# Kernel tuning notes

Measured on AMD Instinct MI355X. Metric: run time of the kernel, lower is better.

## Reference

```python
import jax, jax.numpy as jnp
import numpy as np

MAX_FREQ = 10
CORR_RADIUS = 2
PATCH = 9


def _gelu(x):
    return jax.nn.gelu(x, approximate=False)


def _project(coords, R, C0, f, pp):
    # coords [N,3] -> uv [ncams,N,2], cam-space z [ncams,N]
    d = coords[None, :, :] - C0[:, None, :]
    Xc = jnp.einsum('cij,cnj->cni', R, d)
    z = jnp.maximum(Xc[..., 2:3], 1e-6)
    uv = Xc[..., :2] / z * f[:, None, :] + pp[:, None, :]
    return uv, Xc[..., 2]


def _fourier(x, max_freq):
    freqs = (2.0 ** jnp.arange(max_freq, dtype=x.dtype)) * jnp.pi
    xf = x[..., None] * freqs
    enc = jnp.concatenate([jnp.sin(xf), jnp.cos(xf)], axis=-1)  # [...,D,2F]
    return enc.reshape(enc.shape[:-2] + (x.shape[-1] * 2 * max_freq,))


def _bilinear_time(img, t, gx, gy):
    # img [B,T,C,H,W]; t [B,K] int; gx,gy [B,K,P] normalized grid in [-1,1]
    # grid_sample(align_corners=False, padding_mode='zeros') via direct 4-tap gather
    B, T, C, H, W = img.shape
    x = (gx + 1.0) * 0.5 * W - 0.5
    y = (gy + 1.0) * 0.5 * H - 0.5
    x0 = jnp.floor(x)
    y0 = jnp.floor(y)
    wx = (x - x0)[..., None]
    wy = (y - y0)[..., None]
    x0 = x0.astype(jnp.int32)
    y0 = y0.astype(jnp.int32)
    b = jnp.arange(B)[:, None, None]
    tt = t[:, :, None]

    def tap(yy, xx):
        ok = ((xx >= 0) & (xx < W) & (yy >= 0) & (yy < H))[..., None]
        v = img[b, tt, :, jnp.clip(yy, 0, H - 1), jnp.clip(xx, 0, W - 1)]  # [B,K,P,C]
        return v * ok.astype(v.dtype)

    return (tap(y0, x0) * (1 - wx) * (1 - wy) + tap(y0, x0 + 1) * wx * (1 - wy)
            + tap(y0 + 1, x0) * (1 - wx) * wy + tap(y0 + 1, x0 + 1) * wx * wy)


def _conv2d(x, w, b):
    y = jax.lax.conv_general_dilated(x, w, (1, 1), 'SAME', dimension_numbers=('NCHW', 'OIHW', 'NCHW'))
    return y + b[None, :, None, None]


def _conv3d(x, w, b):
    y = jax.lax.conv_general_dilated(x, w, (1, 1, 1), 'SAME', dimension_numbers=('NCDHW', 'OIDHW', 'NCDHW'))
    return y + b[None, :, None, None, None]


def reference(views, cam_R, cam_center, cam_focal, cam_pp, query_coords, query_time, target_time, cube_scale, v2v_w, v2v_b, lin_vol_w, lin_vol_b, lin_pos_w, lin_pos_b, lin_depth_w, lin_depth_b, conv1_w, conv1_b, conv2_w, conv2_b, conv3_w, conv3_b, mlp1_w, mlp1_b, mlp2_w, mlp2_b, tq_emb, tt_emb, vis_emb_tab, depth_norm_scale, gate_w, gate_b, fus1_w, fus1_b, fus2_w, fus2_b):
    ncams, B, T, C, H, W = views.shape
    K = query_coords.shape[1]
    sizes = jnp.asarray([W, H], dtype=query_coords.dtype)

    # project query points to all cameras
    qflat = query_coords.reshape(-1, 3)
    p2d_flat, zc = _project(qflat, cam_R, cam_center, cam_focal, cam_pp)  # [ncams,BK,2]
    p2d_full = p2d_flat.reshape(ncams, B, K, 2)

    # fourier position embedding
    pp_n = jnp.transpose(p2d_full, (1, 2, 0, 3)) / sizes  # [B,K,ncams,2]
    embed_pos = _fourier(pp_n, MAX_FREQ) @ lin_pos_w.T + lin_pos_b

    # volume embedding: masked multi-camera cube sampling + 3D conv
    cs = 2 * CORR_RADIUS + 1
    P3 = cs ** 3
    row = (jnp.arange(cs, dtype=query_coords.dtype) - CORR_RADIUS) * (cube_scale * 2.0)
    gx3, gy3, gz3 = jnp.meshgrid(row, row, row, indexing='ij')
    xyz = jnp.stack([gx3, gy3, gz3], axis=-1).reshape(-1, 3)  # [P3,3], x outermost
    cube = (query_coords[:, :, None, :] + xyz).reshape(-1, 3)
    pc, _ = _project(cube, cam_R, cam_center, cam_focal, cam_pp)
    pc = pc.reshape(ncams, B, K, P3, 2)
    smps, msks = [], []
    for c in range(ncams):
        g = 2.0 * pc[c] / sizes - 1.0
        m = (g[..., 0] >= -1) & (g[..., 0] <= 1) & (g[..., 1] >= -1) & (g[..., 1] <= 1)
        s = _bilinear_time(views[c], query_time, g[..., 0], g[..., 1])  # [B,K,P3,C]
        smps.append(s)
        msks.append(m)
    vol = jnp.stack(smps)  # [ncams,B,K,P3,C]
    mf = jnp.stack(msks).astype(vol.dtype)[..., None]
    cnt = jnp.maximum(mf.sum(0), 1.0)
    mv = (vol * mf).sum(0) / cnt  # [B,K,P3,C]
    mv = mv.reshape(B, K, cs, cs, cs, C)  # (x,y,z,C)
    mv = jnp.transpose(mv, (0, 1, 5, 4, 3, 2)).reshape(B * K, C, cs, cs, cs)  # [(BK),C,z,y,x]
    mv = _gelu(_conv3d(mv, v2v_w, v2v_b))  # EmbedV2V: Conv3d(3,vdim,3) + GELU
    vd = mv.shape[1]
    mv = mv.reshape(B, K, vd, cs, cs, cs)
    mv = jnp.transpose(mv, (0, 1, 2, 5, 4, 3)).reshape(B, K, vd * P3)  # 'b t 1 (d total)'
    embed_volume = mv @ lin_vol_w.T + lin_vol_b
    embed_volume = jnp.broadcast_to(embed_volume[:, :, None, :], (B, K, ncams, embed_volume.shape[-1]))

    # patch embedding per camera
    lin = jnp.arange(PATCH, dtype=query_coords.dtype)
    gyy, gxx = jnp.meshgrid(lin, lin, indexing='ij')
    offs = jnp.stack([gxx - (PATCH - 1) / 2.0, gyy - (PATCH - 1) / 2.0], axis=-1)  # [P,P,2]
    pats = []
    for c in range(ncams):
        px = p2d_full[c][:, :, None, None, :] + offs  # [B,K,P,P,2]
        g = ((2.0 * px + 1.0) / sizes - 1.0).reshape(B, K, PATCH * PATCH, 2)
        s = _bilinear_time(views[c], query_time, g[..., 0], g[..., 1])  # [B,K,PP,C]
        pats.append(jnp.transpose(s.reshape(B, K, PATCH, PATCH, C), (0, 1, 4, 2, 3)))
    patches = jnp.stack(pats).reshape(ncams * B * K, C, PATCH, PATCH)
    x = _gelu(_conv2d(patches, conv1_w, conv1_b))
    x = _gelu(_conv2d(x, conv2_w, conv2_b))
    x = _gelu(_conv2d(x, conv3_w, conv3_b))
    x = x.reshape(x.shape[0], -1)  # 'b c p q -> b (c p q)'
    x = _gelu(x @ mlp1_w.T + mlp1_b)  # dropout is eval-mode identity
    emb_p = x @ mlp2_w.T + mlp2_b
    embed_patch = jnp.transpose(emb_p.reshape(ncams, B, K, -1), (1, 2, 0, 3))

    E = tq_emb.shape[1]
    embed_qt = jnp.broadcast_to(tq_emb[query_time][:, :, None, :], (B, K, ncams, E))
    embed_tt = jnp.broadcast_to(tt_emb[target_time][:, :, None, :], (B, K, ncams, E))

    # visibility (pinhole in-bounds check with margin=2)
    u = p2d_flat[..., 0]
    v = p2d_flat[..., 1]
    margin = 2.0
    vis = (zc > 0) & (u >= margin) & (u <= W - margin) & (v >= margin) & (v <= H - margin)
    vis = jnp.transpose(vis.reshape(ncams, B, K), (1, 2, 0))  # [B,K,ncams]
    embed_vis = vis_emb_tab[vis.astype(jnp.int32)]

    depths = jnp.linalg.norm(query_coords[:, :, None, :] - cam_center, axis=-1) / (cube_scale * depth_norm_scale[0])
    embed_depth = _fourier(depths[..., None], MAX_FREQ) @ lin_depth_w.T + lin_depth_b

    # gated fusion of 7 terms + fusion MLP
    terms = [embed_pos, embed_volume, embed_patch, embed_qt, embed_tt, embed_vis, embed_depth]
    gates = jax.nn.sigmoid(jnp.concatenate(terms, axis=-1) @ gate_w.T + gate_b)  # [B,K,ncams,7]
    fused = sum(gates[..., i:i + 1] * terms[i] for i in range(len(terms)))
    h = _gelu(fused @ fus1_w.T + fus1_b)
    embed_total = h @ fus2_w.T + fus2_b  # [B,K,ncams,decoder_dim]
    return embed_total, vis


def setup_inputs():
    ks = jax.random.split(jax.random.key(0), 24)
    ncams, B, T, C, H, W = 4, 2, 16, 3, 256, 256
    K, E, MF, cs, P, vdim = 256, 256, 10, 5, 9, 8
    views = jax.random.normal(ks[0], (ncams, B, T, C, H, W), jnp.float32)
    cam_R = jnp.tile(jnp.eye(3, dtype=jnp.float32)[None], (ncams, 1, 1))
    cam_center = jnp.stack([jnp.linspace(-0.5, 0.5, ncams), jnp.linspace(0.5, -0.5, ncams), jnp.full((ncams,), -5.0)], axis=-1).astype(jnp.float32)
    cam_focal = jnp.full((ncams, 2), 200.0, jnp.float32)
    cam_pp = jnp.full((ncams, 2), 128.0, jnp.float32)
    query_coords = jax.random.uniform(ks[1], (B, K, 3), jnp.float32, -1.0, 1.0)
    query_time = jax.random.randint(ks[2], (B, K), 0, T).astype(jnp.int32)
    target_time = jax.random.randint(ks[3], (B, K), 0, T).astype(jnp.int32)
    cube_scale = jnp.float32(0.02)

    def w(k, shape, s=0.02):
        return jax.random.normal(k, shape, jnp.float32) * s

    z = lambda n: jnp.zeros((n,), jnp.float32)
    return dict(
        views=views, cam_R=cam_R, cam_center=cam_center, cam_focal=cam_focal, cam_pp=cam_pp,
        query_coords=query_coords, query_time=query_time, target_time=target_time, cube_scale=cube_scale,
        v2v_w=w(ks[4], (vdim, C, 3, 3, 3)), v2v_b=z(vdim),
        lin_vol_w=w(ks[5], (E, cs ** 3 * vdim)), lin_vol_b=z(E),
        lin_pos_w=w(ks[6], (E, 4 * MF)), lin_pos_b=z(E),
        lin_depth_w=w(ks[7], (E, 2 * MF)), lin_depth_b=z(E),
        conv1_w=w(ks[8], (32, 3, 3, 3)), conv1_b=z(32),
        conv2_w=w(ks[9], (64, 32, 3, 3)), conv2_b=z(64),
        conv3_w=w(ks[10], (128, 64, 3, 3)), conv3_b=z(128),
        mlp1_w=w(ks[11], (2 * E, 128 * P * P)), mlp1_b=z(2 * E),
        mlp2_w=w(ks[12], (E, 2 * E)), mlp2_b=z(E),
        tq_emb=w(ks[13], (T, E), 1.0), tt_emb=w(ks[14], (T, E), 1.0),
        vis_emb_tab=w(ks[15], (2, E), 1.0),
        depth_norm_scale=jnp.array([500.0], jnp.float32),
        gate_w=w(ks[16], (7, 7 * E), 0.01), gate_b=z(7),
        fus1_w=w(ks[17], (4 * E, E)), fus1_b=z(4 * E),
        fus2_w=w(ks[18], (E, 4 * E)), fus2_b=z(E),
    )
```

## Files before the change

kernel.cpp:

```cpp
#include <hip/hip_runtime.h>
#include <hip/hip_bf16.h>

typedef __hip_bfloat16 bf16;
typedef __attribute__((ext_vector_type(8))) short short8;
typedef __attribute__((ext_vector_type(4))) float floatx4;

#define NC 4
#define BB 2
#define TS 16
#define CHN 3
#define HH 256
#define WW 256
#define KQ 256
#define EE 256
#define BKT 512
#define HW 65536
#define IMG_CHUNK 1024
#define NSEG 27
#define CH1 32
#define CH1P 40
#define CH2 64
#define CH2P 72
#define PW 11

#define PB_WCL   32
#define PB_W23   160
#define PB_AUXW  416
#define PB_PROJ  424
#define PB_CUBE  936
#define PB_END   1960

__device__ __forceinline__ float tof(bf16 x){ return __bfloat162float(x); }
__device__ __forceinline__ bf16 tobf(float x){ return __float2bfloat16(x); }
__device__ __forceinline__ float gelu_f(float x){ return 0.5f*x*(1.f+erff(x*0.70710678118654752f)); }
__device__ __forceinline__ float ldx(const void* p, size_t i, int bf){
    return bf ? tof(((const bf16*)p)[i]) : ((const float*)p)[i];
}
__device__ __forceinline__ void gload_lds16(const void* g, void* l){
    __builtin_amdgcn_global_load_lds((const __attribute__((address_space(1))) void*)g,
                                     (__attribute__((address_space(3))) void*)l, 16, 0, 0);
}

struct CvtArgs { const void* src[NSEG]; int dstoff[NSEG]; int cnt[NSEG]; };

struct PrepArgs {
    const void *camF, *camR, *camC, *camP, *qc, *csc;
    const void *c2w, *c3w, *linv, *f1w, *f2w, *m2w, *m1w, *views;
    const int* qtime;
    bf16 *w2cl, *w3cl, *linv_bf, *f1w_bf, *f2w_bf, *m2w_bf, *m1w_bf;
    float *p2d, *visf, *mv;
    void* dout;
    int* flagp;
};

__global__ __launch_bounds__(256) void prep_kernel(CvtArgs ca, float* __restrict__ pool, PrepArgs a)
{
    int bid = blockIdx.x, tid = threadIdx.x;
    int bf = (((const unsigned short*)a.camF)[0] != 0) ? 1 : 0;

    if (bid < PB_WCL){
        for (int s=0; s<NSEG; ++s){
            const void* src = ca.src[s];
            float* d = pool + ca.dstoff[s];
            int n = ca.cnt[s];
            for (int i = bid*256 + tid; i < n; i += PB_WCL*256) d[i] = ldx(src, i, bf);
        }
    } else if (bid < PB_W23){
        int i0 = (bid-PB_WCL)*256 + tid;
        const int stride = (PB_W23-PB_WCL)*256;
        for (int i=i0; i<64*32*9; i+=stride){
            int oc=i/(32*9), r=i%(32*9), ic=r/9, tap=r%9;
            a.w2cl[tap*(64*CH1) + oc*CH1 + ic] = tobf(ldx(a.c2w, i, bf));
        }
        for (int i=i0; i<128*64*9; i+=stride){
            int oc=i/(64*9), r=i%(64*9), ic=r/9, tap=r%9;
            a.w3cl[tap*(128*CH2) + oc*CH2 + ic] = tobf(ldx(a.c3w, i, bf));
        }
    } else if (bid < PB_AUXW){
        int sub = (bid-PB_W23)>>6;
        int i0 = ((bid-PB_W23)&63)*256 + tid;
        const int stride = 64*256;
        if (sub==0){
            for (int i=i0; i<256*1024; i+=stride){
                int r=i>>10, c=i&1023;
                a.linv_bf[i] = tobf(c<1000 ? ldx(a.linv, (size_t)r*1000+c, bf) : 0.f);
            }
        } else if (sub==1){
            for (int i=i0; i<1024*256; i+=stride) a.f1w_bf[i]=tobf(ldx(a.f1w,i,bf));
        } else if (sub==2){
            for (int i=i0; i<256*1024; i+=stride) a.f2w_bf[i]=tobf(ldx(a.f2w,i,bf));
        } else {
            for (int i=i0; i<256*512; i+=stride) a.m2w_bf[i]=tobf(ldx(a.m2w,i,bf));
        }
    } else if (bid < PB_PROJ){
        if (bid==PB_AUXW && tid==0) *a.flagp = bf;
        int idx = (bid-PB_AUXW)*256 + tid;
        if (idx < NC*BKT){
            int c = idx / BKT, bk = idx % BKT;
            float dx = ldx(a.qc,bk*3+0,bf) - ldx(a.camC,c*3+0,bf);
            float dy = ldx(a.qc,bk*3+1,bf) - ldx(a.camC,c*3+1,bf);
            float dz = ldx(a.qc,bk*3+2,bf) - ldx(a.camC,c*3+2,bf);
            float X0 = ldx(a.camR,c*9+0,bf)*dx + ldx(a.camR,c*9+1,bf)*dy + ldx(a.camR,c*9+2,bf)*dz;
            float X1 = ldx(a.camR,c*9+3,bf)*dx + ldx(a.camR,c*9+4,bf)*dy + ldx(a.camR,c*9+5,bf)*dz;
            float X2 = ldx(a.camR,c*9+6,bf)*dx + ldx(a.camR,c*9+7,bf)*dy + ldx(a.camR,c*9+8,bf)*dz;
            float z = fmaxf(X2, 1e-6f);
            float u = X0/z*ldx(a.camF,c*2+0,bf) + ldx(a.camP,c*2+0,bf);
            float v = X1/z*ldx(a.camF,c*2+1,bf) + ldx(a.camP,c*2+1,bf);
            a.p2d[idx*2+0] = u; a.p2d[idx*2+1] = v;
            bool vis = (X2 > 0.f) && (u >= 2.f) && (u <= (float)WW-2.f) && (v >= 2.f) && (v <= (float)HH-2.f);
            a.visf[idx] = vis ? 1.f : 0.f;
            float vv = vis ? 1.f : 0.f;
            size_t vidx = (size_t)BB*KQ*NC*EE + (size_t)bk*NC + c;
            if (bf) ((bf16*)a.dout)[vidx] = tobf(vv);
            else    ((float*)a.dout)[vidx] = vv;
        }
    } else if (bid < PB_CUBE){
        int bk = bid - PB_PROJ;
        int c = tid & 3;
        int pg = tid >> 2;
        int b = bk >> 8;
        float cs2 = ldx(a.csc,0,bf) * 2.f;
        int t = a.qtime[bk];
        float qx0 = ldx(a.qc,bk*3+0,bf);
        float qy0 = ldx(a.qc,bk*3+1,bf);
        float qz0 = ldx(a.qc,bk*3+2,bf);
        float R0=ldx(a.camR,c*9+0,bf), R1=ldx(a.camR,c*9+1,bf), R2=ldx(a.camR,c*9+2,bf);
        float R3=ldx(a.camR,c*9+3,bf), R4=ldx(a.camR,c*9+4,bf), R5=ldx(a.camR,c*9+5,bf);
        float R6=ldx(a.camR,c*9+6,bf), R7=ldx(a.camR,c*9+7,bf), R8=ldx(a.camR,c*9+8,bf);
        float Cx=ldx(a.camC,c*3+0,bf), Cy=ldx(a.camC,c*3+1,bf), Cz=ldx(a.camC,c*3+2,bf);
        float Fx=ldx(a.camF,c*2+0,bf), Fy=ldx(a.camF,c*2+1,bf);
        float Px=ldx(a.camP,c*2+0,bf), Py=ldx(a.camP,c*2+1,bf);
        #pragma unroll
        for (int pass=0; pass<2; ++pass){
            int p = (pass<<6) + pg;
            bool act = p < 125;
            float a0=0.f,a1=0.f,a2=0.f,ms=0.f;
            if (act){
                int i=p/25, j=(p/5)%5, kz=p%5;
                float qx = qx0 + (float)(i-2)*cs2;
                float qy = qy0 + (float)(j-2)*cs2;
                float qz = qz0 + (float)(kz-2)*cs2;
                float dx=qx-Cx, dy=qy-Cy, dz=qz-Cz;
                float X0=R0*dx+R1*dy+R2*dz;
                float X1=R3*dx+R4*dy+R5*dz;
                float X2=R6*dx+R7*dy+R8*dz;
                float z = fmaxf(X2,1e-6f);
                float u = X0/z*Fx+Px, v = X1/z*Fy+Py;
                if (u>=0.f && u<=(float)WW && v>=0.f && v<=(float)HH){
                    ms = 1.f;
                    float x = u-0.5f, y = v-0.5f;
                    float xf = floorf(x), yf = floorf(y);
                    int ix=(int)xf, iy=(int)yf;
                    float wx=x-xf, wy=y-yf;
                    size_t basev = (size_t)((c*BB+b)*TS + t)*CHN*HW;
                    float wxs[2]={1.f-wx,wx}, wys[2]={1.f-wy,wy};
                    #pragma unroll
                    for (int ty=0;ty<2;++ty){
                        int yy=iy+ty; if (yy<0||yy>=HH) continue;
                        #pragma unroll
                        for (int tx=0;tx<2;++tx){
                            int xx=ix+tx; if (xx<0||xx>=WW) continue;
                            float wt=wys[ty]*wxs[tx];
                            size_t o = basev + (size_t)yy*WW+xx;
                            a0 += wt*ldx(a.views,o,bf);
                            a1 += wt*ldx(a.views,o+HW,bf);
                            a2 += wt*ldx(a.views,o+2*HW,bf);
                        }
                    }
                }
            }
            a0 += __shfl_xor(a0,1); a0 += __shfl_xor(a0,2);
            a1 += __shfl_xor(a1,1); a1 += __shfl_xor(a1,2);
            a2 += __shfl_xor(a2,1); a2 += __shfl_xor(a2,2);
            ms += __shfl_xor(ms,1); ms += __shfl_xor(ms,2);
            if (act && c==0){
                float cnt = fmaxf(ms,1.f);
                a.mv[(bk*125+p)*3+0]=a0/cnt;
                a.mv[(bk*125+p)*3+1]=a1/cnt;
                a.mv[(bk*125+p)*3+2]=a2/cnt;
            }
        }
    } else {
        int i0 = (bid-PB_CUBE)*256 + tid;
        const int stride = (PB_END-PB_CUBE)*256;
        const int npair = (512*10368)/2;
        if (bf){
            const unsigned* s = (const unsigned*)a.m1w;
            unsigned* d = (unsigned*)a.m1w_bf;
            for (int i=i0; i<npair; i+=stride) d[i] = s[i];
        } else {
            const float2* s = (const float2*)a.m1w;
            unsigned* d = (unsigned*)a.m1w_bf;
            for (int i=i0; i<npair; i+=stride){
                float2 v = s[i];
                union { bf16 h[2]; unsigned u; } pk;
                pk.h[0]=tobf(v.x); pk.h[1]=tobf(v.y);
                d[i] = pk.u;
            }
        }
    }
}

__global__ __launch_bounds__(128) void vol_conv3d_kernel(
    const float* __restrict__ mv, const float* __restrict__ w,
    const float* __restrict__ bias, bf16* __restrict__ outb)
{
    int bk = blockIdx.x; int tid = threadIdx.x;
    __shared__ float vol[3][7][7][7];
    __shared__ float ws[648];
    __shared__ float bs[8];
    for (int idx=tid; idx<3*343; idx+=128) ((float*)vol)[idx]=0.f;
    for (int idx=tid; idx<648; idx+=128) ws[idx]=w[idx];
    if (tid<8) bs[tid]=bias[tid];
    __syncthreads();
    if (tid<125){
        int i=tid/25, j=(tid/5)%5, kz=tid%5;
        #pragma unroll
        for (int ch=0;ch<3;++ch) vol[ch][kz+1][j+1][i+1] = mv[(bk*125+tid)*3+ch];
    }
    __syncthreads();
    if (tid >= 104 && tid < 128) outb[bk*1024 + 1000 + (tid-104)] = tobf(0.f);
    if (tid<125){
        int w2=tid/25, h2=(tid/5)%5, d2=tid%5;
        for (int oc=0;oc<8;++oc){
            float acc = bs[oc];
            #pragma unroll
            for (int ic=0;ic<3;++ic)
              #pragma unroll
              for (int dz=0;dz<3;++dz)
                #pragma unroll
                for (int dy=0;dy<3;++dy)
                  #pragma unroll
                  for (int dxx=0;dxx<3;++dxx)
                    acc += vol[ic][d2+dz][h2+dy][w2+dxx] * ws[(((oc*3+ic)*3+dz)*3+dy)*3+dxx];
            outb[bk*1024 + oc*125 + tid] = tobf(gelu_f(acc));
        }
    }
}

__global__ __launch_bounds__(256) void patchconv_mfma_kernel(
    const void* __restrict__ views, const float* __restrict__ p2d,
    const int* __restrict__ qtime,
    const float* __restrict__ w1, const float* __restrict__ b1,
    const bf16* __restrict__ w2cl, const float* __restrict__ b2,
    const bf16* __restrict__ w3cl, const float* __restrict__ b3,
    bf16* __restrict__ act_out, int img0, const int* __restrict__ flagp)
{
    int img = img0 + blockIdx.x;
    int c = img>>9, b = (img>>8)&1, k = img&255;
    int bk = b*KQ + k;
    int tid = threadIdx.x;
    int wave = tid>>6, lane = tid&63;

    __shared__ __align__(16) bf16 a2cl[11*PW*CH2P];
    __shared__ __align__(16) bf16 a1cl[11*PW*CH1P];
    __shared__ float w1s[864];
    __shared__ float patch[3][11][11];

    for (int i=tid;i<3*11*11;i+=256) ((float*)patch)[i]=0.f;
    for (int i=tid;i<864;i+=256) w1s[i]=w1[i];
    {
        unsigned int* z1=(unsigned int*)a1cl; int n1 = 11*PW*CH1P/2;
        for (int i=tid;i<n1;i+=256) z1[i]=0u;
        unsigned int* z2=(unsigned int*)a2cl; int n2 = 11*PW*CH2P/2;
        for (int i=tid;i<n2;i+=256) z2[i]=0u;
    }
    __syncthreads();
    if (tid<243){
        int bf = *flagp;
        int ch = tid/81;
        int pp = tid - ch*81;
        float u=p2d[(c*BKT+bk)*2+0], v=p2d[(c*BKT+bk)*2+1];
        int t=qtime[bk];
        int r=pp/9,q=pp%9;
        float x=u+(float)(q-4), y=v+(float)(r-4);
        float xf=floorf(x), yf=floorf(y);
        int ix=(int)xf, iy=(int)yf;
        float wx=x-xf, wy=y-yf;
        size_t base = (size_t)((c*BB+b)*TS+t)*CHN*HW + (size_t)ch*HW;
        float acc=0.f;
        float wxs[2]={1.f-wx,wx}, wys[2]={1.f-wy,wy};
        #pragma unroll
        for (int ty=0;ty<2;++ty){
            int yy=iy+ty; if (yy<0||yy>=HH) continue;
            #pragma unroll
            for (int tx=0;tx<2;++tx){
                int xx=ix+tx; if (xx<0||xx>=WW) continue;
                acc += wys[ty]*wxs[tx]*ldx(views, base + (size_t)yy*WW+xx, bf);
            }
        }
        patch[ch][r+1][q+1]=acc;
    }
    __syncthreads();
    for (int o=tid;o<81*32;o+=256){
        int oc=o&31, pp=o>>5;
        int r=pp/9, q=pp-9*r;
        float acc=b1[oc];
        #pragma unroll
        for (int ic=0;ic<3;++ic)
          #pragma unroll
          for (int dy2=0;dy2<3;++dy2)
            #pragma unroll
            for (int dx2=0;dx2<3;++dx2)
              acc += patch[ic][r+dy2][q+dx2]*w1s[((oc*3+ic)*3+dy2)*3+dx2];
        a1cl[((r+1)*PW+(q+1))*CH1P + oc] = tobf(gelu_f(acc));
    }
    __syncthreads();
    int mrow = lane&15;
    int kgrp = lane>>4;
    int koff = kgrp<<3;
    {
        int baseoff[6];
        #pragma unroll
        for (int m=0;m<6;++m){
            int pos = m*16 + mrow; if (pos>80) pos=80;
            int r=pos/9, q=pos-9*r;
            baseoff[m] = (r*PW+q)*CH1P + koff;
        }
        floatx4 acc2[6];
        #pragma unroll
        for (int m=0;m<6;++m) acc2[m]=(floatx4){0.f,0.f,0.f,0.f};
        int n0 = wave<<4;
        #pragma unroll
        for (int tap=0; tap<9; ++tap){
            int dy=tap/3, dx=tap-3*dy;
            short8 bfrag = *(const short8*)(w2cl + ((size_t)tap*64 + n0 + mrow)*CH1 + koff);
            int toff = (dy*PW+dx)*CH1P;
            #pragma unroll
            for (int m=0;m<6;++m){
                short8 afrag = *(const short8*)&a1cl[baseoff[m]+toff];
                acc2[m] = __builtin_amdgcn_mfma_f32_16x16x32_bf16(afrag, bfrag, acc2[m], 0,0,0);
            }
        }
        int oc = n0 + mrow;
        float bb = b2[oc];
        #pragma unroll
        for (int m=0;m<6;++m){
            #pragma unroll
            for (int rg=0;rg<4;++rg){
                int pos = m*16 + (kgrp<<2)+rg;
                if (pos<=80){
                    int r=pos/9,q=pos-9*r;
                    a2cl[((r+1)*PW+(q+1))*CH2P + oc] = tobf(gelu_f(acc2[m][rg]+bb));
                }
            }
        }
    }
    __syncthreads();
    {
        int baseoff[6];
        #pragma unroll
        for (int m=0;m<6;++m){
            int pos = m*16 + mrow; if (pos>80) pos=80;
            int r=pos/9, q=pos-9*r;
            baseoff[m] = (r*PW+q)*CH2P;
        }
        floatx4 acc3[2][6];
        #pragma unroll
        for (int nt=0;nt<2;++nt)
          #pragma unroll
          for (int m=0;m<6;++m) acc3[nt][m]=(floatx4){0.f,0.f,0.f,0.f};
        int n0 = wave<<5;
        #pragma unroll
        for (int tap=0; tap<9; ++tap){
            int dy=tap/3, dx=tap-3*dy;
            int toff = (dy*PW+dx)*CH2P;
            #pragma unroll
            for (int ks=0;ks<2;++ks){
                int kof2 = (ks<<5) + koff;
                short8 b0 = *(const short8*)(w3cl + ((size_t)tap*128 + n0      + mrow)*CH2 + kof2);
                short8 b1f= *(const short8*)(w3cl + ((size_t)tap*128 + n0 + 16 + mrow)*CH2 + kof2);
                #pragma unroll
                for (int m=0;m<6;++m){
                    short8 af = *(const short8*)&a2cl[baseoff[m]+toff+kof2];
                    acc3[0][m] = __builtin_amdgcn_mfma_f32_16x16x32_bf16(af, b0,  acc3[0][m], 0,0,0);
                    acc3[1][m] = __builtin_amdgcn_mfma_f32_16x16x32_bf16(af, b1f, acc3[1][m], 0,0,0);
                }
            }
        }
        #pragma unroll
        for (int nt=0;nt<2;++nt){
            int oc = n0 + (nt<<4) + mrow;
            float bb = b3[oc];
            #pragma unroll
            for (int m=0;m<6;++m){
                #pragma unroll
                for (int rg=0;rg<4;++rg){
                    int pos = m*16 + (kgrp<<2)+rg;
                    if (pos<=80)
                        act_out[(size_t)blockIdx.x*10368 + oc*81 + pos] = tobf(gelu_f(acc3[nt][m][rg]+bb));
                }
            }
        }
    }
}

template<int OUT>
__global__ __launch_bounds__(256) void gemm_bf16_kernel(
    const bf16* __restrict__ A, const bf16* __restrict__ W, const float* __restrict__ bias,
    float* __restrict__ Cf, void* __restrict__ Cb, int M, int N, int K, int iters,
    const int* __restrict__ flagp)
{
    __shared__ bf16 As[2][64][72];
    __shared__ bf16 Bs[2][64][72];
    int tid = threadIdx.x;
    int wave = tid>>6, lane = tid&63;
    int m0 = blockIdx.y<<6, n0 = blockIdx.x<<6;
    int bfflag = (OUT==3) ? *flagp : 0;
    int lr = tid>>3;
    int lc = (tid&7)<<3;
    const bf16* Ap0 = A + (size_t)(m0+lr)*K    + lc;
    const bf16* Ap1 = A + (size_t)(m0+lr+32)*K + lc;
    const bf16* Wp0 = W + (size_t)(n0+lr)*K    + lc;
    const bf16* Wp1 = W + (size_t)(n0+lr+32)*K + lc;
    uint4 ra0 = *(const uint4*)Ap0;
    uint4 ra1 = *(const uint4*)Ap1;
    uint4 rb0 = *(const uint4*)Wp0;
    uint4 rb1 = *(const uint4*)Wp1;
    floatx4 acc[4];
    #pragma unroll
    for (int j=0;j<4;++j) acc[j] = (floatx4){0.f,0.f,0.f,0.f};
    int arow = (wave<<4) + (lane&15);
    int koff = (lane>>4)<<3;
    int nrow = lane&15;
    *(uint4*)&As[0][lr][lc]    = ra0;
    *(uint4*)&As[0][lr+32][lc] = ra1;
    *(uint4*)&Bs[0][lr][lc]    = rb0;
    *(uint4*)&Bs[0][lr+32][lc] = rb1;
    __syncthreads();
    for (int it=0; it<iters; ++it){
        int cur = it&1;
        if (it+1<iters){
            int off = (it+1)<<6;
            ra0 = *(const uint4*)(Ap0+off);
            ra1 = *(const uint4*)(Ap1+off);
            rb0 = *(const uint4*)(Wp0+off);
            rb1 = *(const uint4*)(Wp1+off);
        }
        #pragma unroll
        for (int kk=0; kk<64; kk+=32){
            short8 af = *(const short8*)&As[cur][arow][kk+koff];
            #pragma unroll
            for (int j=0;j<4;++j){
                short8 bfr = *(const short8*)&Bs[cur][(j<<4)+nrow][kk+koff];
                acc[j] = __builtin_amdgcn_mfma_f32_16x16x32_bf16(af, bfr, acc[j], 0, 0, 0);
            }
        }
        if (it+1<iters){
            __syncthreads();
            int nxt = cur^1;
            *(uint4*)&As[nxt][lr][lc]    = ra0;
            *(uint4*)&As[nxt][lr+32][lc] = ra1;
            *(uint4*)&Bs[nxt][lr][lc]    = rb0;
            *(uint4*)&Bs[nxt][lr+32][lc] = rb1;
            __syncthreads();
        }
    }
    int crow = (wave<<4) + ((lane>>4)<<2);
    int ccol = lane&15;
    #pragma unroll
    for (int j=0;j<4;++j){
        int n = n0 + (j<<4) + ccol;
        if (OUT==1){
            float bb = bias[n];
            #pragma unroll
            for (int r=0;r<4;++r)
                ((bf16*)Cb)[(size_t)(m0+crow+r)*N + n] = tobf(gelu_f(acc[j][r] + bb));
        } else if (OUT==2){
            #pragma unroll
            for (int r=0;r<4;++r)
                Cf[(size_t)(m0+crow+r)*N + n] = acc[j][r];
        } else {
            float bb = bias[n];
            #pragma unroll
            for (int r=0;r<4;++r){
                float v = acc[j][r] + bb;
                size_t ii = (size_t)(m0+crow+r)*N + n;
                if (bfflag) ((bf16*)Cb)[ii] = tobf(v);
                else        ((float*)Cb)[ii] = v;
            }
        }
    }
}

__global__ __launch_bounds__(256) void gemm128_kernel(
    const bf16* __restrict__ A, const bf16* __restrict__ W,
    float* __restrict__ Cf, int N, int K, int kiters_total, int zdiv, int pstride)
{
    __shared__ __align__(16) bf16 As[128][64];
    __shared__ __align__(16) bf16 Bs[128][64];
    int tid = threadIdx.x;
    int wave = tid>>6, lane = tid&63;
    int m0 = blockIdx.y<<7, n0 = blockIdx.x<<7;
    int it0 = (int)(((long)blockIdx.z     * kiters_total) / zdiv);
    int it1 = (int)(((long)(blockIdx.z+1) * kiters_total) / zdiv);
    float* out = Cf + (size_t)blockIdx.z * pstride;
    int srow = (wave<<5) + (lane>>3);
    int scol = (lane&7)<<3;
    const bf16* Ap = A + (size_t)(m0+srow)*K + ((size_t)it0<<6) + scol;
    const bf16* Bp = W + (size_t)(n0+srow)*K + ((size_t)it0<<6) + scol;
    bf16* AsW = &As[wave<<5][0];
    bf16* BsW = &Bs[wave<<5][0];
    floatx4 acc[4][4];
    #pragma unroll
    for (int i=0;i<4;++i)
      #pragma unroll
      for (int j=0;j<4;++j) acc[i][j] = (floatx4){0.f,0.f,0.f,0.f};
    int wm = (wave>>1)<<6, wn = (wave&1)<<6;
    int frow = lane&15, koff = (lane>>4)<<3;
    for (int it=it0; it<it1; ++it){
        size_t off = (size_t)(it-it0)<<6;
        #pragma unroll
        for (int j=0;j<4;++j){
            gload_lds16(Ap + (size_t)(j<<3)*K + off, AsW + (j<<3)*64);
            gload_lds16(Bp + (size_t)(j<<3)*K + off, BsW + (j<<3)*64);
        }
        __syncthreads();
        #pragma unroll
        for (int kk=0;kk<64;kk+=32){
            short8 af[4], bfv[4];
            #pragma unroll
            for (int i=0;i<4;++i) af[i]  = *(const short8*)&As[wm + (i<<4) + frow][kk+koff];
            #pragma unroll
            for (int j=0;j<4;++j) bfv[j] = *(const short8*)&Bs[wn + (j<<4) + frow][kk+koff];
            #pragma unroll
            for (int i=0;i<4;++i)
              #pragma unroll
              for (int j=0;j<4;++j)
                acc[i][j] = __builtin_amdgcn_mfma_f32_16x16x32_bf16(af[i], bfv[j], acc[i][j], 0,0,0);
        }
        __syncthreads();
    }
    int crow = (lane>>4)<<2;
    int ccol = lane&15;
    #pragma unroll
    for (int i=0;i<4;++i){
        int mrow = m0 + wm + (i<<4) + crow;
        #pragma unroll
        for (int j=0;j<4;++j){
            int n = n0 + wn + (j<<4) + ccol;
            #pragma unroll
            for (int r=0;r<4;++r)
                out[(size_t)(mrow+r)*N + n] = acc[i][j][r];
        }
    }
}

__global__ __launch_bounds__(256) void mlp1_fin_kernel(const float* __restrict__ P,
                                                       const float* __restrict__ bias,
                                                       bf16* __restrict__ Cb, int total, int Nmask,
                                                       int pstride){
    for (int i = blockIdx.x*256 + threadIdx.x; i < total; i += gridDim.x*256){
        float s = bias[i & Nmask];
        #pragma unroll
        for (int p=0;p<8;++p) s += P[(size_t)p*pstride + i];
        Cb[i] = tobf(gelu_f(s));
    }
}

__global__ __launch_bounds__(256) void terms_kernel(
    const float* __restrict__ p2d, const float* __restrict__ visf,
    const float* __restrict__ evol, const float* __restrict__ linv_b,
    const float* __restrict__ embp, const float* __restrict__ m2_b,
    const float* __restrict__ lin_pos_w, const float* __restrict__ lin_pos_b,
    const float* __restrict__ lin_depth_w, const float* __restrict__ lin_depth_b,
    const float* __restrict__ tq_emb, const float* __restrict__ tt_emb,
    const float* __restrict__ vis_tab,
    const float* __restrict__ gate_w, const float* __restrict__ gate_b,
    const int* __restrict__ qtime, const int* __restrict__ ttime,
    const float* __restrict__ qc, const float* __restrict__ camC,
    const float* __restrict__ csc, const float* __restrict__ dns,
    bf16* __restrict__ fused)
{
    int row = blockIdx.x;
    int c = row & 3; int bk = row >> 2;
    int tid = threadIdx.x;
    __shared__ float feats[40];
    __shared__ float dfeat[20];
    __shared__ float terms[7][256];
    __shared__ float wred[4][7];
    __shared__ float gates_s[7];
    float u = p2d[(c*BKT+bk)*2+0], v = p2d[(c*BKT+bk)*2+1];
    if (tid < 40){
        int j = tid/20; int rem = tid%20;
        float xval = (j==0) ? u*(1.f/(float)WW) : v*(1.f/(float)HH);
        int fi = rem % 10; bool iscos = (rem >= 10);
        float arg = xval * (float)(1<<fi) * 3.14159265358979323846f;
        feats[tid] = iscos ? cosf(arg) : sinf(arg);
    } else if (tid < 60){
        int rem = tid-40;
        float dx = qc[bk*3+0]-camC[c*3+0];
        float dy = qc[bk*3+1]-camC[c*3+1];
        float dz = qc[bk*3+2]-camC[c*3+2];
        float dep = sqrtf(dx*dx+dy*dy+dz*dz) / (csc[0] * dns[0]);
        int fi = rem % 10; bool iscos = (rem >= 10);
        float arg = dep * (float)(1<<fi) * 3.14159265358979323846f;
        dfeat[rem] = iscos ? cosf(arg) : sinf(arg);
    }
    __syncthreads();
    int e = tid;
    float pos = lin_pos_b[e];
    for (int j2=0;j2<40;++j2) pos += feats[j2]*lin_pos_w[e*40+j2];
    float dep = lin_depth_b[e];
    for (int j2=0;j2<20;++j2) dep += dfeat[j2]*lin_depth_w[e*20+j2];
    float vol = evol[bk*256+e] + linv_b[e];
    int img = (c*BB + (bk>>8))*KQ + (bk&255);
    float pat = embp[(size_t)img*256+e] + m2_b[e];
    int tq = qtime[bk], tt2 = ttime[bk];
    float qtv = tq_emb[tq*256+e];
    float ttv = tt_emb[tt2*256+e];
    int vb = (visf[c*BKT+bk] > 0.5f) ? 1 : 0;
    float viv = vis_tab[vb*256+e];
    terms[0][e]=pos; terms[1][e]=vol; terms[2][e]=pat; terms[3][e]=qtv;
    terms[4][e]=ttv; terms[5][e]=viv; terms[6][e]=dep;
    __syncthreads();
    float pg[7];
    #pragma unroll
    for (int g=0;g<7;++g) pg[g]=0.f;
    for (int j2=tid; j2<1792; j2+=256){
        float cv = ((const float*)terms)[j2];
        #pragma unroll
        for (int g=0;g<7;++g) pg[g] += cv * gate_w[g*1792 + j2];
    }
    #pragma unroll
    for (int g=0;g<7;++g){
        #pragma unroll
        for (int off=32; off>0; off>>=1) pg[g] += __shfl_down(pg[g], off, 64);
    }
    int wave = tid >> 6, lane = tid & 63;
    if (lane==0){
        #pragma unroll
        for (int g=0;g<7;++g) wred[wave][g]=pg[g];
    }
    __syncthreads();
    if (tid < 7){
        float s = wred[0][tid]+wred[1][tid]+wred[2][tid]+wred[3][tid] + gate_b[tid];
        gates_s[tid] = 1.f/(1.f+expf(-s));
    }
    __syncthreads();
    float fv = 0.f;
    #pragma unroll
    for (int g=0;g<7;++g) fv += gates_s[g]*terms[g][e];
    fused[(size_t)row*256 + e] = tobf(fv);
}

extern "C" void kernel_launch(void* const* d_in, const int* in_sizes, int n_in,
                              void* d_out, int out_size, void* d_ws, size_t ws_size,
                              hipStream_t stream) {
    const void* views  = d_in[0];
    const int*  qtime  = (const int*)d_in[6];
    const int*  ttime  = (const int*)d_in[7];

    char* base = (char*)d_ws;
    int*   flag = (int*)base;
    float* pool = (float*)(base + 256);

    CvtArgs ca; int poff = 0; int ns = 0;
    auto add = [&](const void* p, int n)->float* {
        ca.src[ns]=p; ca.dstoff[ns]=poff; ca.cnt[ns]=n;
        float* r = pool+poff; poff += n; ns++; return r;
    };
    float* P_camR = add(d_in[1],36);
    float* P_camC = add(d_in[2],12);
    float* P_camF = add(d_in[3],8);
    float* P_camP = add(d_in[4],8);
    float* P_qc   = add(d_in[5],1536);
    float* P_csc  = add(d_in[8],1);
    float* P_dns  = add(d_in[30],1);
    float* P_v2vw = add(d_in[9],648);
    float* P_v2vb = add(d_in[10],8);
    float* P_linvb= add(d_in[12],256);
    float* P_linpw= add(d_in[13],10240);
    float* P_linpb= add(d_in[14],256);
    float* P_lindw= add(d_in[15],5120);
    float* P_lindb= add(d_in[16],256);
    float* P_c1w  = add(d_in[17],864);
    float* P_c1b  = add(d_in[18],32);
    float* P_c2b  = add(d_in[20],64);
    float* P_c3b  = add(d_in[22],128);
    float* P_m1b  = add(d_in[24],512);
    float* P_m2b  = add(d_in[26],256);
    float* P_tq   = add(d_in[27],4096);
    float* P_tt   = add(d_in[28],4096);
    float* P_vtab = add(d_in[29],512);
    float* P_gw   = add(d_in[31],12544);
    float* P_gb   = add(d_in[32],7);
    float* P_f1b  = add(d_in[34],1024);
    float* P_f2b  = add(d_in[36],256);

    bf16* m1w_bf = (bf16*)(base + 4185600);
    bf16* w2cl   = (bf16*)(base + 14802432);
    bf16* w3cl   = (bf16*)(base + 14839296);
    bf16* linv_bf= (bf16*)(base + 14986752);
    bf16* f1w_bf = (bf16*)(base + 15511040);
    bf16* f2w_bf = (bf16*)(base + 16035328);
    bf16* m2w_bf = (bf16*)(base + 16559616);
    char* pbase  = base + 16821760;
    float* p2d   = (float*)(pbase);
    float* visf  = (float*)(pbase + 16384);
    float* evol  = (float*)(pbase + 24576);
    float* embp  = (float*)(pbase + 548864);
    bf16*  mlp1o_bf = (bf16*)(pbase + 8937472);
    bf16*  fusedb_bf= (bf16*)(pbase + 11034624);
    char*  T     = pbase + 12083200;
    float* mv    = (float*)T;
    bf16*  volf_bf = (bf16*)(T + 786432);
    bf16*  c3act = (bf16*)T;
    bf16*  hbuf_bf = (bf16*)T;
    float* parts = (float*)(pbase + 33316864);

    PrepArgs pa;
    pa.camF=d_in[3]; pa.camR=d_in[1]; pa.camC=d_in[2]; pa.camP=d_in[4];
    pa.qc=d_in[5]; pa.csc=d_in[8];
    pa.c2w=d_in[19]; pa.c3w=d_in[21];
    pa.linv=d_in[11]; pa.f1w=d_in[33]; pa.f2w=d_in[35]; pa.m2w=d_in[25];
    pa.m1w=d_in[23]; pa.views=views; pa.qtime=qtime;
    pa.w2cl=w2cl; pa.w3cl=w3cl; pa.linv_bf=linv_bf; pa.f1w_bf=f1w_bf;
    pa.f2w_bf=f2w_bf; pa.m2w_bf=m2w_bf; pa.m1w_bf=m1w_bf;
    pa.p2d=p2d; pa.visf=visf; pa.mv=mv;
    pa.dout=d_out; pa.flagp=flag;

    prep_kernel<<<PB_END, 256, 0, stream>>>(ca, pool, pa);

    vol_conv3d_kernel<<<BKT, 128, 0, stream>>>(mv, P_v2vw, P_v2vb, volf_bf);
    gemm_bf16_kernel<2><<<dim3(4,8,1), 256, 0, stream>>>(volf_bf, linv_bf, nullptr, evol, nullptr, 512, 256, 1024, 16, nullptr);
    for (int ch=0; ch<2; ++ch){
        int img0 = ch*IMG_CHUNK;
        patchconv_mfma_kernel<<<IMG_CHUNK, 256, 0, stream>>>(views, p2d, qtime, P_c1w, P_c1b,
                                                             w2cl, P_c2b, w3cl, P_c3b, c3act, img0, flag);
        gemm128_kernel<<<dim3(4,8,8), 256, 0, stream>>>(c3act, m1w_bf, parts, 512, 10368, 162, 8, 1024*512);
        mlp1_fin_kernel<<<512, 256, 0, stream>>>(parts, P_m1b, mlp1o_bf + (size_t)img0*512,
                                                 1024*512, 511, 1024*512);
    }
    gemm_bf16_kernel<2><<<dim3(4,32,1), 256, 0, stream>>>(mlp1o_bf, m2w_bf, nullptr, embp, nullptr, 2048, 256, 512, 8, nullptr);
    terms_kernel<<<2048, 256, 0, stream>>>(p2d, visf, evol, P_linvb, embp, P_m2b,
                                           P_linpw, P_linpb, P_lindw, P_lindb,
                                           P_tq, P_tt, P_vtab, P_gw, P_gb,
                                           qtime, ttime, P_qc, P_camC, P_csc, P_dns, fusedb_bf);
    gemm_bf16_kernel<1><<<dim3(16,32,1), 256, 0, stream>>>(fusedb_bf, f1w_bf, P_f1b, nullptr, hbuf_bf, 2048, 1024, 256, 4, nullptr);
    gemm_bf16_kernel<3><<<dim3(4,32,1), 256, 0, stream>>>(hbuf_bf, f2w_bf, P_f2b, nullptr, d_out, 2048, 256, 1024, 16, flag);
    (void)in_sizes; (void)n_in; (void)out_size; (void)ws_size;
}
```

Measured before the change: 467.4 us.

## Fuse conv3d into prep, split-K volume GEMM, single-chunk patch path when workspace allows

Moves the 3D volume convolution into the cube-sampling blocks of the prep kernel, so sampled values stay in shared memory and one launch plus the mv round trip is dropped. The volume linear GEMM becomes split-K over 8 z-slices writing partial sums, which terms_kernel now adds up, to raise the parallelism of a tiny 32-block GEMM. The patchconv/mlp1 path runs as one chunk of 2048 images when the workspace is large enough, halving those launches and widening the gemm128 grid. In exchange the prep blocks use more shared memory and do more work, and there are extra partial-buffer reads.

```diff
diff --git a/kernel.cpp b/kernel.cpp
--- a/kernel.cpp
+++ b/kernel.cpp
@@ -15,8 +15,7 @@
 #define EE 256
 #define BKT 512
 #define HW 65536
-#define IMG_CHUNK 1024
-#define NSEG 27
+#define NSEG 25
 #define CH1 32
 #define CH1P 40
 #define CH2 64
@@ -46,9 +45,11 @@
 struct PrepArgs {
     const void *camF, *camR, *camC, *camP, *qc, *csc;
     const void *c2w, *c3w, *linv, *f1w, *f2w, *m2w, *m1w, *views;
+    const void *v2vw, *v2vb;
     const int* qtime;
     bf16 *w2cl, *w3cl, *linv_bf, *f1w_bf, *f2w_bf, *m2w_bf, *m1w_bf;
-    float *p2d, *visf, *mv;
+    float *p2d, *visf;
+    bf16* volf;
     void* dout;
     int* flagp;
 };
@@ -57,6 +58,9 @@
 {
     int bid = blockIdx.x, tid = threadIdx.x;
     int bf = (((const unsigned short*)a.camF)[0] != 0) ? 1 : 0;
+    __shared__ float s_vol[3][7][7][7];
+    __shared__ float s_ws[648];
+    __shared__ float s_bs[8];
 
     if (bid < PB_WCL){
         for (int s=0; s<NSEG; ++s){
@@ -119,6 +123,10 @@
         int c = tid & 3;
         int pg = tid >> 2;
         int b = bk >> 8;
+        for (int i=tid; i<3*343; i+=256) ((float*)s_vol)[i]=0.f;
+        for (int i=tid; i<648; i+=256) s_ws[i]=ldx(a.v2vw,i,bf);
+        if (tid<8) s_bs[tid]=ldx(a.v2vb,tid,bf);
+        __syncthreads();
         float cs2 = ldx(a.csc,0,bf) * 2.f;
         int t = a.qtime[bk];
         float qx0 = ldx(a.qc,bk*3+0,bf);
@@ -134,9 +142,9 @@
         for (int pass=0; pass<2; ++pass){
             int p = (pass<<6) + pg;
             bool act = p < 125;
+            int i=p/25, j=(p/5)%5, kz=p%5;
             float a0=0.f,a1=0.f,a2=0.f,ms=0.f;
             if (act){
-                int i=p/25, j=(p/5)%5, kz=p%5;
                 float qx = qx0 + (float)(i-2)*cs2;
                 float qy = qy0 + (float)(j-2)*cs2;
                 float qz = qz0 + (float)(kz-2)*cs2;
@@ -175,9 +183,27 @@
             ms += __shfl_xor(ms,1); ms += __shfl_xor(ms,2);
             if (act && c==0){
                 float cnt = fmaxf(ms,1.f);
-                a.mv[(bk*125+p)*3+0]=a0/cnt;
-                a.mv[(bk*125+p)*3+1]=a1/cnt;
-                a.mv[(bk*125+p)*3+2]=a2/cnt;
+                s_vol[0][kz+1][j+1][i+1]=a0/cnt;
+                s_vol[1][kz+1][j+1][i+1]=a1/cnt;
+                s_vol[2][kz+1][j+1][i+1]=a2/cnt;
+            }
+        }
+        __syncthreads();
+        if (tid >= 104 && tid < 128) a.volf[bk*1024 + 1000 + (tid-104)] = tobf(0.f);
+        if (tid < 125){
+            int w2=tid/25, h2=(tid/5)%5, d2=tid%5;
+            for (int oc=0;oc<8;++oc){
+                float acc = s_bs[oc];
+                #pragma unroll
+                for (int ic=0;ic<3;++ic)
+                  #pragma unroll
+                  for (int dz=0;dz<3;++dz)
+                    #pragma unroll
+                    for (int dy=0;dy<3;++dy)
+                      #pragma unroll
+                      for (int dxx=0;dxx<3;++dxx)
+                        acc += s_vol[ic][d2+dz][h2+dy][w2+dxx] * s_ws[(((oc*3+ic)*3+dz)*3+dy)*3+dxx];
+                a.volf[bk*1024 + oc*125 + tid] = tobf(gelu_f(acc));
             }
         }
     } else {
@@ -201,43 +227,6 @@
     }
 }
 
-__global__ __launch_bounds__(128) void vol_conv3d_kernel(
-    const float* __restrict__ mv, const float* __restrict__ w,
-    const float* __restrict__ bias, bf16* __restrict__ outb)
-{
-    int bk = blockIdx.x; int tid = threadIdx.x;
-    __shared__ float vol[3][7][7][7];
-    __shared__ float ws[648];
-    __shared__ float bs[8];
-    for (int idx=tid; idx<3*343; idx+=128) ((float*)vol)[idx]=0.f;
-    for (int idx=tid; idx<648; idx+=128) ws[idx]=w[idx];
-    if (tid<8) bs[tid]=bias[tid];
-    __syncthreads();
-    if (tid<125){
-        int i=tid/25, j=(tid/5)%5, kz=tid%5;
-        #pragma unroll
-        for (int ch=0;ch<3;++ch) vol[ch][kz+1][j+1][i+1] = mv[(bk*125+tid)*3+ch];
-    }
-    __syncthreads();
-    if (tid >= 104 && tid < 128) outb[bk*1024 + 1000 + (tid-104)] = tobf(0.f);
-    if (tid<125){
-        int w2=tid/25, h2=(tid/5)%5, d2=tid%5;
-        for (int oc=0;oc<8;++oc){
-            float acc = bs[oc];
-            #pragma unroll
-            for (int ic=0;ic<3;++ic)
-              #pragma unroll
-              for (int dz=0;dz<3;++dz)
-                #pragma unroll
-                for (int dy=0;dy<3;++dy)
-                  #pragma unroll
-                  for (int dxx=0;dxx<3;++dxx)
-                    acc += vol[ic][d2+dz][h2+dy][w2+dxx] * ws[(((oc*3+ic)*3+dz)*3+dy)*3+dxx];
-            outb[bk*1024 + oc*125 + tid] = tobf(gelu_f(acc));
-        }
-    }
-}
-
 __global__ __launch_bounds__(256) void patchconv_mfma_kernel(
     const void* __restrict__ views, const float* __restrict__ p2d,
     const int* __restrict__ qtime,
@@ -399,20 +388,21 @@
 __global__ __launch_bounds__(256) void gemm_bf16_kernel(
     const bf16* __restrict__ A, const bf16* __restrict__ W, const float* __restrict__ bias,
     float* __restrict__ Cf, void* __restrict__ Cb, int M, int N, int K, int iters,
-    const int* __restrict__ flagp)
+    int pstride, const int* __restrict__ flagp)
 {
     __shared__ bf16 As[2][64][72];
     __shared__ bf16 Bs[2][64][72];
     int tid = threadIdx.x;
     int wave = tid>>6, lane = tid&63;
     int m0 = blockIdx.y<<6, n0 = blockIdx.x<<6;
+    int kt0 = blockIdx.z*iters;
     int bfflag = (OUT==3) ? *flagp : 0;
     int lr = tid>>3;
     int lc = (tid&7)<<3;
-    const bf16* Ap0 = A + (size_t)(m0+lr)*K    + lc;
-    const bf16* Ap1 = A + (size_t)(m0+lr+32)*K + lc;
-    const bf16* Wp0 = W + (size_t)(n0+lr)*K    + lc;
-    const bf16* Wp1 = W + (size_t)(n0+lr+32)*K + lc;
+    const bf16* Ap0 = A + (size_t)(m0+lr)*K    + (kt0<<6) + lc;
+    const bf16* Ap1 = A + (size_t)(m0+lr+32)*K + (kt0<<6) + lc;
+    const bf16* Wp0 = W + (size_t)(n0+lr)*K    + (kt0<<6) + lc;
+    const bf16* Wp1 = W + (size_t)(n0+lr+32)*K + (kt0<<6) + lc;
     uint4 ra0 = *(const uint4*)Ap0;
     uint4 ra1 = *(const uint4*)Ap1;
     uint4 rb0 = *(const uint4*)Wp0;
@@ -467,9 +457,10 @@
             for (int r=0;r<4;++r)
                 ((bf16*)Cb)[(size_t)(m0+crow+r)*N + n] = tobf(gelu_f(acc[j][r] + bb));
         } else if (OUT==2){
+            float* out = Cf + (size_t)blockIdx.z * pstride;
             #pragma unroll
             for (int r=0;r<4;++r)
-                Cf[(size_t)(m0+crow+r)*N + n] = acc[j][r];
+                out[(size_t)(m0+crow+r)*N + n] = acc[j][r];
         } else {
             float bb = bias[n];
             #pragma unroll
@@ -560,7 +551,7 @@
 
 __global__ __launch_bounds__(256) void terms_kernel(
     const float* __restrict__ p2d, const float* __restrict__ visf,
-    const float* __restrict__ evol, const float* __restrict__ linv_b,
+    const float* __restrict__ lvp, const float* __restrict__ linv_b,
     const float* __restrict__ embp, const float* __restrict__ m2_b,
     const float* __restrict__ lin_pos_w, const float* __restrict__ lin_pos_b,
     const float* __restrict__ lin_depth_w, const float* __restrict__ lin_depth_b,
@@ -603,7 +594,9 @@
     for (int j2=0;j2<40;++j2) pos += feats[j2]*lin_pos_w[e*40+j2];
     float dep = lin_depth_b[e];
     for (int j2=0;j2<20;++j2) dep += dfeat[j2]*lin_depth_w[e*20+j2];
-    float vol = evol[bk*256+e] + linv_b[e];
+    float vol = linv_b[e];
+    #pragma unroll
+    for (int p=0;p<8;++p) vol += lvp[(size_t)p*(512*256) + bk*256+e];
     int img = (c*BB + (bk>>8))*KQ + (bk&255);
     float pat = embp[(size_t)img*256+e] + m2_b[e];
     int tq = qtime[bk], tt2 = ttime[bk];
@@ -667,8 +660,6 @@
     float* P_qc   = add(d_in[5],1536);
     float* P_csc  = add(d_in[8],1);
     float* P_dns  = add(d_in[30],1);
-    float* P_v2vw = add(d_in[9],648);
-    float* P_v2vb = add(d_in[10],8);
     float* P_linvb= add(d_in[12],256);
     float* P_linpw= add(d_in[13],10240);
     float* P_linpb= add(d_in[14],256);
@@ -695,49 +686,54 @@
     bf16* f1w_bf = (bf16*)(base + 15511040);
     bf16* f2w_bf = (bf16*)(base + 16035328);
     bf16* m2w_bf = (bf16*)(base + 16559616);
-    char* pbase  = base + 16821760;
-    float* p2d   = (float*)(pbase);
-    float* visf  = (float*)(pbase + 16384);
-    float* evol  = (float*)(pbase + 24576);
-    float* embp  = (float*)(pbase + 548864);
-    bf16*  mlp1o_bf = (bf16*)(pbase + 8937472);
-    bf16*  fusedb_bf= (bf16*)(pbase + 11034624);
-    char*  T     = pbase + 12083200;
-    float* mv    = (float*)T;
-    bf16*  volf_bf = (bf16*)(T + 786432);
-    bf16*  c3act = (bf16*)T;
-    bf16*  hbuf_bf = (bf16*)T;
-    float* parts = (float*)(pbase + 33316864);
+    float* p2d   = (float*)(base + 16821760);
+    float* visf  = (float*)(base + 16838144);
+    bf16*  volf_bf = (bf16*)(base + 16846336);
+    float* lvparts = (float*)(base + 17894912);
+    float* embp  = (float*)(base + 22089216);
+    bf16*  mlp1o_bf = (bf16*)(base + 24186368);
+    bf16*  fusedb_bf= (bf16*)(base + 26283520);
+    int NCH = (ws_size >= 103353856ull) ? 1 : 2;
+    int MCH = 2048 / NCH;
+    bf16*  c3act   = (bf16*)(base + 27332096);
+    bf16*  hbuf_bf = (bf16*)(base + 27332096);
+    float* parts   = (float*)(base + 27332096 + (size_t)MCH*10368*2);
 
     PrepArgs pa;
     pa.camF=d_in[3]; pa.camR=d_in[1]; pa.camC=d_in[2]; pa.camP=d_in[4];
     pa.qc=d_in[5]; pa.csc=d_in[8];
     pa.c2w=d_in[19]; pa.c3w=d_in[21];
     pa.linv=d_in[11]; pa.f1w=d_in[33]; pa.f2w=d_in[35]; pa.m2w=d_in[25];
-    pa.m1w=d_in[23]; pa.views=views; pa.qtime=qtime;
+    pa.m1w=d_in[23]; pa.views=views;
+    pa.v2vw=d_in[9]; pa.v2vb=d_in[10];
+    pa.qtime=qtime;
     pa.w2cl=w2cl; pa.w3cl=w3cl; pa.linv_bf=linv_bf; pa.f1w_bf=f1w_bf;
     pa.f2w_bf=f2w_bf; pa.m2w_bf=m2w_bf; pa.m1w_bf=m1w_bf;
-    pa.p2d=p2d; pa.visf=visf; pa.mv=mv;
+    pa.p2d=p2d; pa.visf=visf; pa.volf=volf_bf;
     pa.dout=d_out; pa.flagp=flag;
 
     prep_kernel<<<PB_END, 256, 0, stream>>>(ca, pool, pa);
 
-    vol_conv3d_kernel<<<BKT, 128, 0, stream>>>(mv, P_v2vw, P_v2vb, volf_bf);
-    gemm_bf16_kernel<2><<<dim3(4,8,1), 256, 0, stream>>>(volf_bf, linv_bf, nullptr, evol, nullptr, 512, 256, 1024, 16, nullptr);
-    for (int ch=0; ch<2; ++ch){
-        int img0 = ch*IMG_CHUNK;
-        patchconv_mfma_kernel<<<IMG_CHUNK, 256, 0, stream>>>(views, p2d, qtime, P_c1w, P_c1b,
-                                                             w2cl, P_c2b, w3cl, P_c3b, c3act, img0, flag);
-        gemm128_kernel<<<dim3(4,8,8), 256, 0, stream>>>(c3act, m1w_bf, parts, 512, 10368, 162, 8, 1024*512);
+    gemm_bf16_kernel<2><<<dim3(4,8,8), 256, 0, stream>>>(volf_bf, linv_bf, nullptr, lvparts, nullptr,
+                                                         512, 256, 1024, 2, 512*256, nullptr);
+    for (int ch=0; ch<NCH; ++ch){
+        int img0 = ch*MCH;
+        patchconv_mfma_kernel<<<MCH, 256, 0, stream>>>(views, p2d, qtime, P_c1w, P_c1b,
+                                                       w2cl, P_c2b, w3cl, P_c3b, c3act, img0, flag);
+        gemm128_kernel<<<dim3(4, MCH/128, 8), 256, 0, stream>>>(c3act, m1w_bf, parts,
+                                                                512, 10368, 162, 8, MCH*512);
         mlp1_fin_kernel<<<512, 256, 0, stream>>>(parts, P_m1b, mlp1o_bf + (size_t)img0*512,
-                                                 1024*512, 511, 1024*512);
-    }
-    gemm_bf16_kernel<2><<<dim3(4,32,1), 256, 0, stream>>>(mlp1o_bf, m2w_bf, nullptr, embp, nullptr, 2048, 256, 512, 8, nullptr);
-    terms_kernel<<<2048, 256, 0, stream>>>(p2d, visf, evol, P_linvb, embp, P_m2b,
+                                                 MCH*512, 511, MCH*512);
+    }
+    gemm_bf16_kernel<2><<<dim3(4,32,1), 256, 0, stream>>>(mlp1o_bf, m2w_bf, nullptr, embp, nullptr,
+                                                          2048, 256, 512, 8, 0, nullptr);
+    terms_kernel<<<2048, 256, 0, stream>>>(p2d, visf, lvparts, P_linvb, embp, P_m2b,
                                            P_linpw, P_linpb, P_lindw, P_lindb,
                                            P_tq, P_tt, P_vtab, P_gw, P_gb,
                                            qtime, ttime, P_qc, P_camC, P_csc, P_dns, fusedb_bf);
-    gemm_bf16_kernel<1><<<dim3(16,32,1), 256, 0, stream>>>(fusedb_bf, f1w_bf, P_f1b, nullptr, hbuf_bf, 2048, 1024, 256, 4, nullptr);
-    gemm_bf16_kernel<3><<<dim3(4,32,1), 256, 0, stream>>>(hbuf_bf, f2w_bf, P_f2b, nullptr, d_out, 2048, 256, 1024, 16, flag);
-    (void)in_sizes; (void)n_in; (void)out_size; (void)ws_size;
-}
+    gemm_bf16_kernel<1><<<dim3(16,32,1), 256, 0, stream>>>(fusedb_bf, f1w_bf, P_f1b, nullptr, hbuf_bf,
+                                                           2048, 1024, 256, 4, 0, nullptr);
+    gemm_bf16_kernel<3><<<dim3(4,32,1), 256, 0, stream>>>(hbuf_bf, f2w_bf, P_f2b, nullptr, d_out,
+                                                          2048, 256, 1024, 16, 0, flag);
+    (void)in_sizes; (void)n_in; (void)out_size;
+}
```

After: 414.6 us. 11.3% less time.
